# Performance work log

Measured on AMD Instinct MI355X. Metric: run time of the kernel, lower is better.

Reference implementation:

```python
import jax, jax.numpy as jnp
import numpy as np

B, N, C, H = 4, 1024, 768, 12
D = C // H  # head_dim = 64


def setup_inputs() -> dict:
    key = jax.random.key(0)
    ks = jax.random.split(key, 6)
    x = jax.random.normal(ks[0], (B, N, C), dtype=jnp.float32)
    W_qkv = jax.random.normal(ks[1], (C, 3 * C), dtype=jnp.float32) * (C ** -0.5)
    b_qkv = jnp.zeros((3 * C,), dtype=jnp.float32)
    scale = jnp.asarray(D ** -0.5, dtype=jnp.float32)       # learnable scalar in torch
    riem_scale = jnp.asarray(D ** -0.5, dtype=jnp.float32)  # learnable scalar in torch
    # 1x1 Conv2d(2H -> H) == channel-mixing matrix [H, 2H] + bias [H]
    W_conv = jax.random.normal(ks[2], (H, 2 * H), dtype=jnp.float32) * ((2 * H) ** -0.5)
    b_conv = jnp.zeros((H,), dtype=jnp.float32)
    W_proj = jax.random.normal(ks[3], (C, C), dtype=jnp.float32) * (C ** -0.5)
    b_proj = jnp.zeros((C,), dtype=jnp.float32)
    return dict(x=x, W_qkv=W_qkv, b_qkv=b_qkv, scale=scale, riem_scale=riem_scale,
                W_conv=W_conv, b_conv=b_conv, W_proj=W_proj, b_proj=b_proj)


def reference(x, W_qkv, b_qkv, scale, riem_scale, W_conv, b_conv, W_proj, b_proj):
    Bx, Nx, Cx = x.shape
    Hh = W_conv.shape[0]
    d = Cx // Hh
    # qkv projection -> [3, B, H, N, d]
    qkv = (x @ W_qkv + b_qkv).reshape(Bx, Nx, 3, Hh, d).transpose(2, 0, 3, 1, 4)
    q, k, v = qkv[0], qkv[1], qkv[2]
    # standard scaled dot-product scores [B, H, N, N]
    attn = jnp.einsum('bhnd,bhmd->bhnm', q, k) * scale
    # covariance-Frobenius (Riemannian) scores: center along feature dim, then
    # <q_c q_c^T, k_c k_c^T>_F = (q_c . k_c)^2 pairwise
    qc = q - q.mean(axis=-1, keepdims=True)
    kc = k - k.mean(axis=-1, keepdims=True)
    attn_riem = jnp.einsum('bhnd,bhmd->bhnm', qc, kc) ** 2 * riem_scale
    # concat along head/channel dim -> [B, 2H, N, N], then 1x1 conv channel mix
    cat = jnp.concatenate([attn, attn_riem], axis=1)
    mixed = jnp.einsum('bcnm,oc->bonm', cat, W_conv) + b_conv[None, :, None, None]
    attn_ = jax.nn.softmax(mixed, axis=-1)  # [B, H, N, N]
    out = jnp.einsum('bhnm,bhmd->bhnd', attn_, v)
    out = out.transpose(0, 2, 1, 3).reshape(Bx, Nx, Cx)
    return out @ W_proj + b_proj, attn_
```

## Files before the change

kernel.cpp:

```cpp
#include <hip/hip_runtime.h>
#include <cstddef>
#include <cstdint>

#define B_ 4
#define N_ 1024
#define C_ 768
#define H_ 12
#define D_ 64

typedef __attribute__((ext_vector_type(8))) short bf16x8;
typedef __attribute__((ext_vector_type(4))) short s16x4;
typedef __attribute__((ext_vector_type(4))) float f32x4;
typedef __attribute__((ext_vector_type(2))) float f32x2;

#define MFMA16(a_, b_, c_) __builtin_amdgcn_mfma_f32_16x16x32_bf16((a_), (b_), (c_), 0, 0, 0)
#define GLLDS16(gp_, lp_) __builtin_amdgcn_global_load_lds( \
    (const __attribute__((address_space(1))) unsigned int*)(gp_), \
    (__attribute__((address_space(3))) unsigned int*)(lp_), 16, 0, 0)

__device__ __forceinline__ unsigned short f2bf(float f) {
  unsigned int u = __float_as_uint(f);
  u += 0x7fffu + ((u >> 16) & 1u);
  return (unsigned short)(u >> 16);
}
__device__ __forceinline__ float bf2f(unsigned short b) {
  return __uint_as_float(((unsigned int)b) << 16);
}

__global__ __launch_bounds__(256) void k_prep(const float* __restrict__ x,
                                              short* __restrict__ xhi, short* __restrict__ xlo,
                                              const float* __restrict__ Wq,
                                              short* __restrict__ Wthi, short* __restrict__ Wtlo,
                                              const float* __restrict__ Wp,
                                              short* __restrict__ Wpthi, short* __restrict__ Wptlo) {
  __shared__ float tile[32][33];
  const int f = blockIdx.x;
  const int t = threadIdx.x;
  if (f < 1536) {
    const size_t i = ((size_t)f * 256 + t) * 8;
    float4 a = *reinterpret_cast<const float4*>(&x[i]);
    float4 b = *reinterpret_cast<const float4*>(&x[i + 4]);
    float v[8] = {a.x, a.y, a.z, a.w, b.x, b.y, b.z, b.w};
    bf16x8 hi, lo;
#pragma unroll
    for (int j = 0; j < 8; ++j) {
      unsigned short h = f2bf(v[j]);
      hi[j] = (short)h;
      lo[j] = (short)f2bf(v[j] - bf2f(h));
    }
    *reinterpret_cast<bf16x8*>(&xhi[i]) = hi;
    *reinterpret_cast<bf16x8*>(&xlo[i]) = lo;
    return;
  }
  const float* W;
  short *Thi, *Tlo;
  int Kd, Nn, bx, by;
  if (f < 3264) {
    const int local = f - 1536;
    W = Wq; Thi = Wthi; Tlo = Wtlo; Kd = 768; Nn = 2304;
    bx = local % 72; by = local / 72;
  } else {
    const int local = f - 3264;
    W = Wp; Thi = Wpthi; Tlo = Wptlo; Kd = 768; Nn = 768;
    bx = local % 24; by = local / 24;
  }
  const int k0 = by * 32, n0 = bx * 32;
  const int r = t >> 3, cq = (t & 7) * 4;
  float4 v = *reinterpret_cast<const float4*>(&W[(size_t)(k0 + r) * Nn + n0 + cq]);
  tile[r][cq + 0] = v.x; tile[r][cq + 1] = v.y;
  tile[r][cq + 2] = v.z; tile[r][cq + 3] = v.w;
  __syncthreads();
  const int nrow = t >> 3, kq = (t & 7) * 4;
  s16x4 hi, lo;
#pragma unroll
  for (int i = 0; i < 4; ++i) {
    float fv = tile[kq + i][nrow];
    unsigned short h = f2bf(fv);
    hi[i] = (short)h;
    lo[i] = (short)f2bf(fv - bf2f(h));
  }
  *reinterpret_cast<s16x4*>(&Thi[(size_t)(n0 + nrow) * Kd + k0 + kq]) = hi;
  *reinterpret_cast<s16x4*>(&Tlo[(size_t)(n0 + nrow) * Kd + k0 + kq]) = lo;
}

__global__ __launch_bounds__(256) void k_fold(const float* __restrict__ Wc,
                                              const float* __restrict__ scale_p,
                                              const float* __restrict__ riem_p,
                                              float* __restrict__ Wfold) {
  const int t = threadIdx.x;
  const float scale = scale_p[0], riem = riem_p[0];
  for (int i = t; i < 288; i += 256)
    Wfold[i] = Wc[i] * (((i % 24) < 12) ? scale : riem);
}

__global__ __launch_bounds__(256) void k_gemm(const short* __restrict__ Ahi,
                                              const short* __restrict__ Alo,
                                              const short* __restrict__ Bhi,
                                              const short* __restrict__ Blo,
                                              const float* __restrict__ bias,
                                              float* __restrict__ Cout,
                                              int M, int Nn, int Kd) {
  __shared__ __align__(16) short sA[2][128 * 32];
  __shared__ __align__(16) short sB[2][64 * 32];
  const int tid = threadIdx.x;
  const int wv = tid >> 6, l = tid & 63;
  const int lr = l & 15, lg = l >> 4;
  const int row0 = blockIdx.y * 128;
  const int col0 = blockIdx.x * 64;
  const int wr = (wv >> 1) * 64;
  const int wc = (wv & 1) * 32;
  const int ar = tid >> 2, ac = tid & 3;
  f32x4 acc[4][2];
#pragma unroll
  for (int i = 0; i < 4; ++i)
#pragma unroll
    for (int j = 0; j < 2; ++j) acc[i][j] = (f32x4){0.f, 0.f, 0.f, 0.f};

  for (int k0 = 0; k0 < Kd; k0 += 32) {
#pragma unroll
    for (int j = 0; j < 2; ++j) {
      const int row = j * 64 + ar;
      const int cc = ac ^ ((row >> 1) & 3);
      const size_t so = (size_t)(row0 + row) * Kd + k0 + cc * 8;
      GLLDS16(Ahi + so, &sA[0][(j * 256 + (wv << 6)) * 8]);
      GLLDS16(Alo + so, &sA[1][(j * 256 + (wv << 6)) * 8]);
    }
    {
      const int row = ar;
      const int cc = ac ^ ((row >> 1) & 3);
      const size_t so = (size_t)(col0 + row) * Kd + k0 + cc * 8;
      GLLDS16(Bhi + so, &sB[0][(wv << 6) * 8]);
      GLLDS16(Blo + so, &sB[1][(wv << 6) * 8]);
    }
    __syncthreads();
    bf16x8 afh[4], afl[4], bfh[2], bfl[2];
#pragma unroll
    for (int ti = 0; ti < 4; ++ti) {
      const int row = wr + ti * 16 + lr;
      const int pc = lg ^ ((row >> 1) & 3);
      afh[ti] = *reinterpret_cast<const bf16x8*>(&sA[0][row * 32 + pc * 8]);
      afl[ti] = *reinterpret_cast<const bf16x8*>(&sA[1][row * 32 + pc * 8]);
    }
#pragma unroll
    for (int tj = 0; tj < 2; ++tj) {
      const int row = wc + tj * 16 + lr;
      const int pc = lg ^ ((row >> 1) & 3);
      bfh[tj] = *reinterpret_cast<const bf16x8*>(&sB[0][row * 32 + pc * 8]);
      bfl[tj] = *reinterpret_cast<const bf16x8*>(&sB[1][row * 32 + pc * 8]);
    }
#pragma unroll
    for (int ti = 0; ti < 4; ++ti)
#pragma unroll
      for (int tj = 0; tj < 2; ++tj) {
        acc[ti][tj] = MFMA16(afh[ti], bfh[tj], acc[ti][tj]);
        acc[ti][tj] = MFMA16(afl[ti], bfh[tj], acc[ti][tj]);
        acc[ti][tj] = MFMA16(afh[ti], bfl[tj], acc[ti][tj]);
      }
    __syncthreads();
  }
#pragma unroll
  for (int ti = 0; ti < 4; ++ti)
#pragma unroll
    for (int tj = 0; tj < 2; ++tj) {
      const int col = col0 + wc + tj * 16 + lr;
      const float bb = bias[col];
#pragma unroll
      for (int r = 0; r < 4; ++r) {
        const int row = row0 + wr + ti * 16 + lg * 4 + r;
        Cout[(size_t)row * Nn + col] = acc[ti][tj][r] + bb;
      }
    }
}

__global__ __launch_bounds__(256) void k_gemm128(const short* __restrict__ Ahi,
                                                 const short* __restrict__ Alo,
                                                 const short* __restrict__ Bhi,
                                                 const short* __restrict__ Blo,
                                                 const float* __restrict__ bias,
                                                 float* __restrict__ Cout,
                                                 int M, int Nn, int Kd) {
  __shared__ __align__(16) short sA[2][128 * 32];
  __shared__ __align__(16) short sB[2][128 * 32];
  const int tid = threadIdx.x;
  const int wv = tid >> 6, l = tid & 63;
  const int lr = l & 15, lg = l >> 4;
  const int row0 = blockIdx.y * 128;
  const int col0 = blockIdx.x * 128;
  const int wr = (wv >> 1) * 64;
  const int wc = (wv & 1) * 64;
  const int ar = tid >> 2, ac = tid & 3;
  f32x4 acc[4][4];
#pragma unroll
  for (int i = 0; i < 4; ++i)
#pragma unroll
    for (int j = 0; j < 4; ++j) acc[i][j] = (f32x4){0.f, 0.f, 0.f, 0.f};

  for (int k0 = 0; k0 < Kd; k0 += 32) {
#pragma unroll
    for (int j = 0; j < 2; ++j) {
      const int row = j * 64 + ar;
      const int cc = ac ^ ((row >> 1) & 3);
      const size_t ao = (size_t)(row0 + row) * Kd + k0 + cc * 8;
      const size_t bo = (size_t)(col0 + row) * Kd + k0 + cc * 8;
      GLLDS16(Ahi + ao, &sA[0][(j * 256 + (wv << 6)) * 8]);
      GLLDS16(Alo + ao, &sA[1][(j * 256 + (wv << 6)) * 8]);
      GLLDS16(Bhi + bo, &sB[0][(j * 256 + (wv << 6)) * 8]);
      GLLDS16(Blo + bo, &sB[1][(j * 256 + (wv << 6)) * 8]);
    }
    __syncthreads();
    bf16x8 afh[4], afl[4], bfh[4], bfl[4];
#pragma unroll
    for (int ti = 0; ti < 4; ++ti) {
      const int row = wr + ti * 16 + lr;
      const int pc = lg ^ ((row >> 1) & 3);
      afh[ti] = *reinterpret_cast<const bf16x8*>(&sA[0][row * 32 + pc * 8]);
      afl[ti] = *reinterpret_cast<const bf16x8*>(&sA[1][row * 32 + pc * 8]);
    }
#pragma unroll
    for (int tj = 0; tj < 4; ++tj) {
      const int row = wc + tj * 16 + lr;
      const int pc = lg ^ ((row >> 1) & 3);
      bfh[tj] = *reinterpret_cast<const bf16x8*>(&sB[0][row * 32 + pc * 8]);
      bfl[tj] = *reinterpret_cast<const bf16x8*>(&sB[1][row * 32 + pc * 8]);
    }
#pragma unroll
    for (int ti = 0; ti < 4; ++ti)
#pragma unroll
      for (int tj = 0; tj < 4; ++tj) {
        acc[ti][tj] = MFMA16(afh[ti], bfh[tj], acc[ti][tj]);
        acc[ti][tj] = MFMA16(afl[ti], bfh[tj], acc[ti][tj]);
        acc[ti][tj] = MFMA16(afh[ti], bfl[tj], acc[ti][tj]);
      }
    __syncthreads();
  }
#pragma unroll
  for (int ti = 0; ti < 4; ++ti)
#pragma unroll
    for (int tj = 0; tj < 4; ++tj) {
      const int col = col0 + wc + tj * 16 + lr;
      const float bb = bias[col];
#pragma unroll
      for (int r = 0; r < 4; ++r) {
        const int row = row0 + wr + ti * 16 + lg * 4 + r;
        Cout[(size_t)row * Nn + col] = acc[ti][tj][r] + bb;
      }
    }
}

__global__ __launch_bounds__(256) void k_qkv_post(const float* __restrict__ qkvf,
                                                  short* __restrict__ Qhi, short* __restrict__ Qlo,
                                                  short* __restrict__ KChi, short* __restrict__ KClo,
                                                  short* __restrict__ Vt,
                                                  float* __restrict__ Qm, float* __restrict__ Km) {
  __shared__ unsigned short lvh[64][33];
  const int b = blockIdx.z, h = blockIdx.y, n0 = blockIdx.x * 32;
  const int t = threadIdx.x;
  const int row = t >> 3, d0 = (t & 7) * 8;
  const int n = n0 + row;
  const float* base = qkvf + ((size_t)(b * 1024 + n)) * 2304 + h * 64 + d0;
  const size_t qko = ((size_t)(b * H_ + h) * N_ + n) * D_ + d0;

#pragma unroll
  for (int part = 0; part < 2; ++part) {
    float4 a = *reinterpret_cast<const float4*>(base + part * 768);
    float4 c = *reinterpret_cast<const float4*>(base + part * 768 + 4);
    float v[8] = {a.x, a.y, a.z, a.w, c.x, c.y, c.z, c.w};
    float s = v[0] + v[1] + v[2] + v[3] + v[4] + v[5] + v[6] + v[7];
#pragma unroll
    for (int off = 1; off < 8; off <<= 1) s += __shfl_xor(s, off);
    const float mean = s * (1.0f / 64.0f);
    if ((t & 7) == 0) (part ? Km : Qm)[(size_t)(b * H_ + h) * N_ + n] = mean;
    const float sub = part ? mean : 0.0f;
    bf16x8 hi, lo;
#pragma unroll
    for (int j = 0; j < 8; ++j) {
      const float fv = v[j] - sub;
      unsigned short hh = f2bf(fv);
      hi[j] = (short)hh;
      lo[j] = (short)f2bf(fv - bf2f(hh));
    }
    *reinterpret_cast<bf16x8*>((part ? KChi : Qhi) + qko) = hi;
    *reinterpret_cast<bf16x8*>((part ? KClo : Qlo) + qko) = lo;
  }
  {
    float4 a = *reinterpret_cast<const float4*>(base + 1536);
    float4 c = *reinterpret_cast<const float4*>(base + 1536 + 4);
    float v[8] = {a.x, a.y, a.z, a.w, c.x, c.y, c.z, c.w};
#pragma unroll
    for (int j = 0; j < 8; ++j) lvh[d0 + j][row] = f2bf(v[j]);
  }
  __syncthreads();
  const int d = t >> 2, c = t & 3;
  bf16x8 vh;
#pragma unroll
  for (int i = 0; i < 8; ++i) vh[i] = (short)lvh[d][c * 8 + i];
  const size_t vo = ((size_t)(b * H_ + h) * D_ + d) * N_ + n0 + c * 8;
  *reinterpret_cast<bf16x8*>(Vt + vo) = vh;
}

__global__ __launch_bounds__(256, 2) void k_scores(
    const short* __restrict__ Qhi, const short* __restrict__ Qlo,
    const short* __restrict__ KChi, const short* __restrict__ KClo,
    const float* __restrict__ Qm, const float* __restrict__ Km,
    const float* __restrict__ Wfold, float* __restrict__ logits,
    float2* __restrict__ stats) {
  __shared__ __align__(16) short sCh[2][32 * 64];
  __shared__ __align__(16) short sCl[2][32 * 64];
  __shared__ float sQm[12][64];
  __shared__ float sKm[12][32];

  const int t = threadIdx.x;
  const int b = blockIdx.z;
  const int n0 = blockIdx.y * 64, m0 = blockIdx.x * 32;
  const int wv = t >> 6, l = t & 63;
  const int lr = l & 15, lg = l >> 4;
  const size_t bh0 = (size_t)b * H_;

  for (int i = t; i < 768; i += 256)
    sQm[i >> 6][i & 63] = Qm[(bh0 + (i >> 6)) * N_ + n0 + (i & 63)];
  for (int i = t; i < 384; i += 256)
    sKm[i >> 5][i & 31] = Km[(bh0 + (i >> 5)) * N_ + m0 + (i & 31)];

  const int srow = t >> 3;
  const int scs = (t & 7) ^ (srow & 7);
  const size_t csrc = (bh0 * N_ + m0 + srow) * D_ + scs * 8;
  const size_t hstep = (size_t)N_ * D_;
  const int nb = n0 + wv * 16;
  const size_t qsrc = (bh0 * N_ + nb + lr) * D_ + lg * 8;

  GLLDS16(KChi + csrc, &sCh[0][wv * 512]);
  GLLDS16(KClo + csrc, &sCl[0][wv * 512]);
  bf16x8 qh0 = *reinterpret_cast<const bf16x8*>(Qhi + qsrc);
  bf16x8 qh1 = *reinterpret_cast<const bf16x8*>(Qhi + qsrc + 32);
  bf16x8 ql0 = *reinterpret_cast<const bf16x8*>(Qlo + qsrc);
  bf16x8 ql1 = *reinterpret_cast<const bf16x8*>(Qlo + qsrc + 32);

  f32x2 aA01[12], aA23[12], aB01[12], aB23[12];
#pragma unroll
  for (int o = 0; o < 12; ++o) {
    aA01[o] = (f32x2){0.f, 0.f}; aA23[o] = (f32x2){0.f, 0.f};
    aB01[o] = (f32x2){0.f, 0.f}; aB23[o] = (f32x2){0.f, 0.f};
  }

  const int browA = lr, browB = 16 + lr;
  const int aiA0 = browA * 64 + ((lg + 0) ^ (browA & 7)) * 8;
  const int aiA1 = browA * 64 + ((lg + 4) ^ (browA & 7)) * 8;
  const int aiB0 = browB * 64 + ((lg + 0) ^ (browB & 7)) * 8;
  const int aiB1 = browB * 64 + ((lg + 4) ^ (browB & 7)) * 8;
  __syncthreads();

  int buf = 0;
#pragma unroll 2
  for (int h = 0; h < H_; ++h) {
    bf16x8 nqh0, nqh1, nql0, nql1;
    if (h < 11) {
      const size_t cs = csrc + (size_t)(h + 1) * hstep;
      GLLDS16(KChi + cs, &sCh[buf ^ 1][wv * 512]);
      GLLDS16(KClo + cs, &sCl[buf ^ 1][wv * 512]);
      const size_t qs = qsrc + (size_t)(h + 1) * hstep;
      nqh0 = *reinterpret_cast<const bf16x8*>(Qhi + qs);
      nqh1 = *reinterpret_cast<const bf16x8*>(Qhi + qs + 32);
      nql0 = *reinterpret_cast<const bf16x8*>(Qlo + qs);
      nql1 = *reinterpret_cast<const bf16x8*>(Qlo + qs + 32);
    }
    const bf16x8 chA0 = *reinterpret_cast<const bf16x8*>(&sCh[buf][aiA0]);
    const bf16x8 chA1 = *reinterpret_cast<const bf16x8*>(&sCh[buf][aiA1]);
    const bf16x8 clA0 = *reinterpret_cast<const bf16x8*>(&sCl[buf][aiA0]);
    const bf16x8 clA1 = *reinterpret_cast<const bf16x8*>(&sCl[buf][aiA1]);
    const bf16x8 chB0 = *reinterpret_cast<const bf16x8*>(&sCh[buf][aiB0]);
    const bf16x8 chB1 = *reinterpret_cast<const bf16x8*>(&sCh[buf][aiB1]);
    const bf16x8 clB0 = *reinterpret_cast<const bf16x8*>(&sCl[buf][aiB0]);
    const bf16x8 clB1 = *reinterpret_cast<const bf16x8*>(&sCl[buf][aiB1]);

    f32x4 uaA = {0.f, 0.f, 0.f, 0.f}, ubA = {0.f, 0.f, 0.f, 0.f};
    f32x4 uaB = {0.f, 0.f, 0.f, 0.f}, ubB = {0.f, 0.f, 0.f, 0.f};
    uaA = MFMA16(qh0, chA0, uaA);  ubA = MFMA16(qh1, chA1, ubA);
    uaB = MFMA16(qh0, chB0, uaB);  ubB = MFMA16(qh1, chB1, ubB);
    uaA = MFMA16(qh0, clA0, uaA);  ubA = MFMA16(qh1, clA1, ubA);
    uaB = MFMA16(qh0, clB0, uaB);  ubB = MFMA16(qh1, clB1, ubB);
    uaA = MFMA16(ql0, chA0, uaA);  ubA = MFMA16(ql1, chA1, ubA);
    uaB = MFMA16(ql0, chB0, uaB);  ubB = MFMA16(ql1, chB1, ubB);

    const float4 qm4 = *reinterpret_cast<const float4*>(&sQm[h][wv * 16 + lg * 4]);
    const float kmA = 64.0f * sKm[h][lr];
    const float kmB = 64.0f * sKm[h][16 + lr];
    const f32x2 qm01 = {qm4.x, qm4.y};
    const f32x2 qm23 = {qm4.z, qm4.w};
    const f32x2 uA01 = {uaA[0] + ubA[0], uaA[1] + ubA[1]};
    const f32x2 uA23 = {uaA[2] + ubA[2], uaA[3] + ubA[3]};
    const f32x2 uB01 = {uaB[0] + ubB[0], uaB[1] + ubB[1]};
    const f32x2 uB23 = {uaB[2] + ubB[2], uaB[3] + ubB[3]};
    const f32x2 svA01 = kmA * qm01 + uA01;
    const f32x2 svA23 = kmA * qm23 + uA23;
    const f32x2 svB01 = kmB * qm01 + uB01;
    const f32x2 svB23 = kmB * qm23 + uB23;
    const f32x2 u2A01 = uA01 * uA01;
    const f32x2 u2A23 = uA23 * uA23;
    const f32x2 u2B01 = uB01 * uB01;
    const f32x2 u2B23 = uB23 * uB23;
#pragma unroll
    for (int o = 0; o < 12; ++o) {
      const float we = Wfold[o * 24 + h];
      const float wr = Wfold[o * 24 + 12 + h];
      aA01[o] = aA01[o] + we * svA01 + wr * u2A01;
      aA23[o] = aA23[o] + we * svA23 + wr * u2A23;
      aB01[o] = aB01[o] + we * svB01 + wr * u2B01;
      aB23[o] = aB23[o] + we * svB23 + wr * u2B23;
    }
    __syncthreads();
    buf ^= 1;
    if (h < 11) { qh0 = nqh0; qh1 = nqh1; ql0 = nql0; ql1 = nql1; }
  }

#pragma unroll
  for (int o = 0; o < 12; ++o) {
    float* dst = &logits[((bh0 + o) * N_ + nb) * N_ + m0 + lr];
    dst[(size_t)(lg * 4 + 0) * N_] = aA01[o][0];
    dst[(size_t)(lg * 4 + 1) * N_] = aA01[o][1];
    dst[(size_t)(lg * 4 + 2) * N_] = aA23[o][0];
    dst[(size_t)(lg * 4 + 3) * N_] = aA23[o][1];
    dst[(size_t)(lg * 4 + 0) * N_ + 16] = aB01[o][0];
    dst[(size_t)(lg * 4 + 1) * N_ + 16] = aB01[o][1];
    dst[(size_t)(lg * 4 + 2) * N_ + 16] = aB23[o][0];
    dst[(size_t)(lg * 4 + 3) * N_ + 16] = aB23[o][1];
  }
#pragma unroll
  for (int o = 0; o < 12; ++o) {
    float avA[4] = {aA01[o][0], aA01[o][1], aA23[o][0], aA23[o][1]};
    float avB[4] = {aB01[o][0], aB01[o][1], aB23[o][0], aB23[o][1]};
    float M4[4], S4[4];
#pragma unroll
    for (int r = 0; r < 4; ++r) {
      float mxA = avA[r], mxB = avB[r];
      mxA = fmaxf(mxA, __shfl_xor(mxA, 1)); mxB = fmaxf(mxB, __shfl_xor(mxB, 1));
      mxA = fmaxf(mxA, __shfl_xor(mxA, 2)); mxB = fmaxf(mxB, __shfl_xor(mxB, 2));
      mxA = fmaxf(mxA, __shfl_xor(mxA, 4)); mxB = fmaxf(mxB, __shfl_xor(mxB, 4));
      mxA = fmaxf(mxA, __shfl_xor(mxA, 8)); mxB = fmaxf(mxB, __shfl_xor(mxB, 8));
      const float M = fmaxf(mxA, mxB);
      float eA = __expf(avA[r] - M);
      float eB = __expf(avB[r] - M);
      float e = eA + eB;
      e += __shfl_xor(e, 1);
      e += __shfl_xor(e, 2);
      e += __shfl_xor(e, 4);
      e += __shfl_xor(e, 8);
      M4[r] = M; S4[r] = e;
    }
    if (lr < 4) {
      const int n = nb + lg * 4 + lr;
      stats[(((size_t)b * 12 + o) * 32 + blockIdx.x) * 1024 + n] = make_float2(M4[lr], S4[lr]);
    }
  }
}

__global__ __launch_bounds__(256) void k_pvsm(float* __restrict__ attn,
                                              const float2* __restrict__ stats,
                                              const short* __restrict__ Vt,
                                              short* __restrict__ ohi,
                                              short* __restrict__ olo) {
  __shared__ __align__(16) short sPhi[64 * 64];
  __shared__ __align__(16) short sPlo[64 * 64];
  __shared__ __align__(16) short sV[2][64 * 64];
  __shared__ float sM[64], sIS[64];
  const int flat = blockIdx.x + blockIdx.y * 16 + blockIdx.z * 192;
  const int swz = (flat & 7) * 96 + (flat >> 3);
  const int b = swz / 192;
  const int rem = swz - b * 192;
  const int o = rem >> 4;
  const int n0 = (rem & 15) * 64;
  const int bo = b * H_ + o;
  const int t = threadIdx.x;
  const int wv = t >> 6, l = t & 63;
  const int lr = l & 15, lg = l >> 4;
  const int nsub = wv * 16;

  const int vr0 = t >> 3, vr1 = vr0 + 32;
  const int vc0 = (t & 7) ^ (vr0 & 7);
  const int vc1 = (t & 7) ^ (vr1 & 7);
  const size_t vbase = (size_t)bo * D_ * N_;
  const size_t vs0 = vbase + (size_t)vr0 * N_ + vc0 * 8;
  const size_t vs1 = vbase + (size_t)vr1 * N_ + vc1 * 8;

  GLLDS16(Vt + vs0, &sV[0][(wv * 64) * 8]);
  GLLDS16(Vt + vs1, &sV[0][(wv * 64 + 256) * 8]);

  if (t < 64) {
    const int n = n0 + t;
    const float2* sp = stats + ((size_t)bo * 32) * 1024 + n;
    float M = -3.0e38f, S = 0.f;
    for (int seg = 0; seg < 32; ++seg) {
      const float2 p = sp[(size_t)seg * 1024];
      if (p.x > M) {
        S = S * __expf(M - p.x) + p.y;
        M = p.x;
      } else {
        S += p.y * __expf(p.x - M);
      }
    }
    sM[t] = M;
    sIS[t] = 1.0f / S;
  }

  const int prow = t >> 3, c0 = (t & 7) * 8;
  float* lrowA = attn + ((size_t)bo * N_ + n0 + prow) * N_;
  float* lrowB = attn + ((size_t)bo * N_ + n0 + prow + 32) * N_;
  const int pofsA = prow * 64 + (((t & 7) ^ (prow & 7)) * 8);
  const int pofsB = pofsA + 32 * 64;

  const int arow = nsub + lr;
  const int ai0 = arow * 64 + (((lg + 0) ^ (arow & 7)) * 8);
  const int ai1 = arow * 64 + (((lg + 4) ^ (arow & 7)) * 8);

  f32x4 acc[4];
#pragma unroll
  for (int dt = 0; dt < 4; ++dt) acc[dt] = (f32x4){0.f, 0.f, 0.f, 0.f};
  __syncthreads();

  for (int mc = 0; mc < 16; ++mc) {
    const int m0 = mc * 64;
    if (mc < 15) {
      const int nb2 = (mc + 1) & 1;
      GLLDS16(Vt + vs0 + m0 + 64, &sV[nb2][(wv * 64) * 8]);
      GLLDS16(Vt + vs1 + m0 + 64, &sV[nb2][(wv * 64 + 256) * 8]);
    }
    const float MrA = sM[prow], iSA = sIS[prow];
    const float MrB = sM[prow + 32], iSB = sIS[prow + 32];
    float4 laA = *reinterpret_cast<const float4*>(&lrowA[m0 + c0]);
    float4 lbA = *reinterpret_cast<const float4*>(&lrowA[m0 + c0 + 4]);
    float4 laB = *reinterpret_cast<const float4*>(&lrowB[m0 + c0]);
    float4 lbB = *reinterpret_cast<const float4*>(&lrowB[m0 + c0 + 4]);
    float pA[8], pB[8];
    pA[0] = __expf(laA.x - MrA) * iSA; pA[1] = __expf(laA.y - MrA) * iSA;
    pA[2] = __expf(laA.z - MrA) * iSA; pA[3] = __expf(laA.w - MrA) * iSA;
    pA[4] = __expf(lbA.x - MrA) * iSA; pA[5] = __expf(lbA.y - MrA) * iSA;
    pA[6] = __expf(lbA.z - MrA) * iSA; pA[7] = __expf(lbA.w - MrA) * iSA;
    pB[0] = __expf(laB.x - MrB) * iSB; pB[1] = __expf(laB.y - MrB) * iSB;
    pB[2] = __expf(laB.z - MrB) * iSB; pB[3] = __expf(laB.w - MrB) * iSB;
    pB[4] = __expf(lbB.x - MrB) * iSB; pB[5] = __expf(lbB.y - MrB) * iSB;
    pB[6] = __expf(lbB.z - MrB) * iSB; pB[7] = __expf(lbB.w - MrB) * iSB;
    float4 oaA = {pA[0], pA[1], pA[2], pA[3]};
    float4 obA = {pA[4], pA[5], pA[6], pA[7]};
    float4 oaB = {pB[0], pB[1], pB[2], pB[3]};
    float4 obB = {pB[4], pB[5], pB[6], pB[7]};
    *reinterpret_cast<float4*>(&lrowA[m0 + c0]) = oaA;
    *reinterpret_cast<float4*>(&lrowA[m0 + c0 + 4]) = obA;
    *reinterpret_cast<float4*>(&lrowB[m0 + c0]) = oaB;
    *reinterpret_cast<float4*>(&lrowB[m0 + c0 + 4]) = obB;
    bf16x8 phiA, ploA, phiB, ploB;
#pragma unroll
    for (int j = 0; j < 8; ++j) {
      unsigned short hA = f2bf(pA[j]);
      phiA[j] = (short)hA;
      ploA[j] = (short)f2bf(pA[j] - bf2f(hA));
      unsigned short hB = f2bf(pB[j]);
      phiB[j] = (short)hB;
      ploB[j] = (short)f2bf(pB[j] - bf2f(hB));
    }
    *reinterpret_cast<bf16x8*>(&sPhi[pofsA]) = phiA;
    *reinterpret_cast<bf16x8*>(&sPlo[pofsA]) = ploA;
    *reinterpret_cast<bf16x8*>(&sPhi[pofsB]) = phiB;
    *reinterpret_cast<bf16x8*>(&sPlo[pofsB]) = ploB;
    __syncthreads();

    const int cur = mc & 1;
    const bf16x8 pah0 = *reinterpret_cast<const bf16x8*>(&sPhi[ai0]);
    const bf16x8 pah1 = *reinterpret_cast<const bf16x8*>(&sPhi[ai1]);
    const bf16x8 pal0 = *reinterpret_cast<const bf16x8*>(&sPlo[ai0]);
    const bf16x8 pal1 = *reinterpret_cast<const bf16x8*>(&sPlo[ai1]);
#pragma unroll
    for (int dt = 0; dt < 4; ++dt) {
      const int drow = dt * 16 + lr;
      const bf16x8 vh0 = *reinterpret_cast<const bf16x8*>(&sV[cur][drow * 64 + (((lg + 0) ^ (drow & 7)) * 8)]);
      const bf16x8 vh1 = *reinterpret_cast<const bf16x8*>(&sV[cur][drow * 64 + (((lg + 4) ^ (drow & 7)) * 8)]);
      acc[dt] = MFMA16(pah0, vh0, acc[dt]);
      acc[dt] = MFMA16(pal0, vh0, acc[dt]);
      acc[dt] = MFMA16(pah1, vh1, acc[dt]);
      acc[dt] = MFMA16(pal1, vh1, acc[dt]);
    }
    __syncthreads();
  }
#pragma unroll
  for (int dt = 0; dt < 4; ++dt) {
    const int d = dt * 16 + lr;
#pragma unroll
    for (int r = 0; r < 4; ++r) {
      const int n = n0 + nsub + lg * 4 + r;
      const float val = acc[dt][r];
      const unsigned short hh = f2bf(val);
      const size_t oo = (size_t)(b * 1024 + n) * 768 + o * 64 + d;
      ohi[oo] = (short)hh;
      olo[oo] = (short)f2bf(val - bf2f(hh));
    }
  }
}

extern "C" void kernel_launch(void* const* d_in, const int* in_sizes, int n_in,
                              void* d_out, int out_size, void* d_ws, size_t ws_size,
                              hipStream_t stream) {
  (void)in_sizes; (void)n_in; (void)out_size; (void)ws_size;
  const float* x      = (const float*)d_in[0];
  const float* W_qkv  = (const float*)d_in[1];
  const float* b_qkv  = (const float*)d_in[2];
  const float* scale  = (const float*)d_in[3];
  const float* riem   = (const float*)d_in[4];
  const float* W_conv = (const float*)d_in[5];
  const float* W_proj = (const float*)d_in[7];
  const float* b_proj = (const float*)d_in[8];

  float* out_final = (float*)d_out;
  float* attn_out  = out_final + (size_t)B_ * N_ * C_;

  char* w = (char*)d_ws;
  short* xhi  = (short*)w;
  short* xlo  = xhi + 3145728;
  short* Wthi = (short*)(w + 12582912);
  short* Wtlo = Wthi + 1769472;
  short* Wpthi = (short*)(w + 19660800);
  short* Wptlo = Wpthi + 589824;
  float* qkvf = (float*)(w + 22020096);
  short* Qhi  = (short*)(w + 59768832);
  short* Qlo  = Qhi + 3145728;
  short* KChi = Qlo + 3145728;
  short* KClo = KChi + 3145728;
  short* Vt = xhi;
  float* Wfold = (float*)Wthi;
  float* Qm = (float*)((char*)Wthi + 8192);
  float* Km = (float*)((char*)Wthi + 8192 + 196608);
  float2* stats = (float2*)((char*)qkvf + 12582912);

  short* ohi = Qhi;
  short* olo = Qlo;

  k_prep<<<dim3(3840), 256, 0, stream>>>(x, xhi, xlo, W_qkv, Wthi, Wtlo, W_proj, Wpthi, Wptlo);
  k_gemm128<<<dim3(18, 32), 256, 0, stream>>>(xhi, xlo, Wthi, Wtlo, b_qkv, qkvf, 4096, 2304, 768);
  k_fold<<<dim3(1), 256, 0, stream>>>(W_conv, scale, riem, Wfold);
  k_qkv_post<<<dim3(32, 12, 4), 256, 0, stream>>>(qkvf, Qhi, Qlo, KChi, KClo, Vt, Qm, Km);
  k_scores<<<dim3(32, 16, 4), 256, 0, stream>>>(Qhi, Qlo, KChi, KClo, Qm, Km, Wfold, attn_out, stats);
  k_pvsm<<<dim3(16, 12, 4), 256, 0, stream>>>(attn_out, stats, Vt, ohi, olo);
  k_gemm<<<dim3(12, 32), 256, 0, stream>>>(ohi, olo, Wpthi, Wptlo, b_proj, out_final, 4096, 768, 768);
}
```

Before: 348.4 us.

## Store mixed logits as fp16 offsets in attn buffer, reconstruct in-place in PV

The logits kernel now writes each logit as an fp16 value relative to its per-segment row max into the first half of each attn row, halving logit write and read traffic. The PV/softmax kernel stores per-segment max offsets in fp16 in LDS, reads the fp16 logits, and iterates column chunks in reverse so the fp32 probabilities written back to the same row do not overwrite unread fp16 data. The probability store is also moved after the barrier. This risks precision loss from fp16 logit storage and depends on ordering across threads to avoid in-place aliasing hazards.

```diff
diff --git a/kernel.cpp b/kernel.cpp
--- a/kernel.cpp
+++ b/kernel.cpp
@@ -25,6 +25,17 @@
 }
 __device__ __forceinline__ float bf2f(unsigned short b) {
   return __uint_as_float(((unsigned int)b) << 16);
+}
+__device__ __forceinline__ short f2h(float f) {
+  _Float16 h = (_Float16)f;
+  short s;
+  __builtin_memcpy(&s, &h, 2);
+  return s;
+}
+__device__ __forceinline__ float h2f(short s) {
+  _Float16 h;
+  __builtin_memcpy(&h, &s, 2);
+  return (float)h;
 }
 
 __global__ __launch_bounds__(256) void k_prep(const float* __restrict__ x,
@@ -414,18 +425,6 @@
 
 #pragma unroll
   for (int o = 0; o < 12; ++o) {
-    float* dst = &logits[((bh0 + o) * N_ + nb) * N_ + m0 + lr];
-    dst[(size_t)(lg * 4 + 0) * N_] = aA01[o][0];
-    dst[(size_t)(lg * 4 + 1) * N_] = aA01[o][1];
-    dst[(size_t)(lg * 4 + 2) * N_] = aA23[o][0];
-    dst[(size_t)(lg * 4 + 3) * N_] = aA23[o][1];
-    dst[(size_t)(lg * 4 + 0) * N_ + 16] = aB01[o][0];
-    dst[(size_t)(lg * 4 + 1) * N_ + 16] = aB01[o][1];
-    dst[(size_t)(lg * 4 + 2) * N_ + 16] = aB23[o][0];
-    dst[(size_t)(lg * 4 + 3) * N_ + 16] = aB23[o][1];
-  }
-#pragma unroll
-  for (int o = 0; o < 12; ++o) {
     float avA[4] = {aA01[o][0], aA01[o][1], aA23[o][0], aA23[o][1]};
     float avB[4] = {aB01[o][0], aB01[o][1], aB23[o][0], aB23[o][1]};
     float M4[4], S4[4];
@@ -446,6 +445,12 @@
       e += __shfl_xor(e, 8);
       M4[r] = M; S4[r] = e;
     }
+#pragma unroll
+    for (int r = 0; r < 4; ++r) {
+      short* rowp = (short*)(logits + ((bh0 + o) * N_ + nb + lg * 4 + r) * (size_t)N_);
+      rowp[m0 + lr] = f2h(avA[r] - M4[r]);
+      rowp[m0 + 16 + lr] = f2h(avB[r] - M4[r]);
+    }
     if (lr < 4) {
       const int n = nb + lg * 4 + lr;
       stats[(((size_t)b * 12 + o) * 32 + blockIdx.x) * 1024 + n] = make_float2(M4[lr], S4[lr]);
@@ -461,7 +466,8 @@
   __shared__ __align__(16) short sPhi[64 * 64];
   __shared__ __align__(16) short sPlo[64 * 64];
   __shared__ __align__(16) short sV[2][64 * 64];
-  __shared__ float sM[64], sIS[64];
+  __shared__ float sIS[64];
+  __shared__ short sMseg16[64 * 32];
   const int flat = blockIdx.x + blockIdx.y * 16 + blockIdx.z * 192;
   const int swz = (flat & 7) * 96 + (flat >> 3);
   const int b = swz / 192;
@@ -481,8 +487,8 @@
   const size_t vs0 = vbase + (size_t)vr0 * N_ + vc0 * 8;
   const size_t vs1 = vbase + (size_t)vr1 * N_ + vc1 * 8;
 
-  GLLDS16(Vt + vs0, &sV[0][(wv * 64) * 8]);
-  GLLDS16(Vt + vs1, &sV[0][(wv * 64 + 256) * 8]);
+  GLLDS16(Vt + vs0 + 960, &sV[1][(wv * 64) * 8]);
+  GLLDS16(Vt + vs1 + 960, &sV[1][(wv * 64 + 256) * 8]);
 
   if (t < 64) {
     const int n = n0 + t;
@@ -497,8 +503,9 @@
         S += p.y * __expf(p.x - M);
       }
     }
-    sM[t] = M;
     sIS[t] = 1.0f / S;
+    for (int seg = 0; seg < 32; ++seg)
+      sMseg16[t * 32 + seg] = f2h(sp[(size_t)seg * 1024].x - M);
   }
 
   const int prow = t >> 3, c0 = (t & 7) * 8;
@@ -516,28 +523,41 @@
   for (int dt = 0; dt < 4; ++dt) acc[dt] = (f32x4){0.f, 0.f, 0.f, 0.f};
   __syncthreads();
 
-  for (int mc = 0; mc < 16; ++mc) {
+  for (int mc = 15; mc >= 0; --mc) {
     const int m0 = mc * 64;
-    if (mc < 15) {
-      const int nb2 = (mc + 1) & 1;
-      GLLDS16(Vt + vs0 + m0 + 64, &sV[nb2][(wv * 64) * 8]);
-      GLLDS16(Vt + vs1 + m0 + 64, &sV[nb2][(wv * 64 + 256) * 8]);
-    }
-    const float MrA = sM[prow], iSA = sIS[prow];
-    const float MrB = sM[prow + 32], iSB = sIS[prow + 32];
-    float4 laA = *reinterpret_cast<const float4*>(&lrowA[m0 + c0]);
-    float4 lbA = *reinterpret_cast<const float4*>(&lrowA[m0 + c0 + 4]);
-    float4 laB = *reinterpret_cast<const float4*>(&lrowB[m0 + c0]);
-    float4 lbB = *reinterpret_cast<const float4*>(&lrowB[m0 + c0 + 4]);
+    if (mc > 0) {
+      const int nb2 = (mc - 1) & 1;
+      GLLDS16(Vt + vs0 + m0 - 64, &sV[nb2][(wv * 64) * 8]);
+      GLLDS16(Vt + vs1 + m0 - 64, &sV[nb2][(wv * 64 + 256) * 8]);
+    }
+    const int sidx = mc * 2 + ((t & 7) >> 2);
+    const float ofsA = h2f(sMseg16[prow * 32 + sidx]);
+    const float ofsB = h2f(sMseg16[(prow + 32) * 32 + sidx]);
+    const float iSA = sIS[prow], iSB = sIS[prow + 32];
+    const bf16x8 rA = *reinterpret_cast<const bf16x8*>(&((const short*)lrowA)[m0 + c0]);
+    const bf16x8 rB = *reinterpret_cast<const bf16x8*>(&((const short*)lrowB)[m0 + c0]);
     float pA[8], pB[8];
-    pA[0] = __expf(laA.x - MrA) * iSA; pA[1] = __expf(laA.y - MrA) * iSA;
-    pA[2] = __expf(laA.z - MrA) * iSA; pA[3] = __expf(laA.w - MrA) * iSA;
-    pA[4] = __expf(lbA.x - MrA) * iSA; pA[5] = __expf(lbA.y - MrA) * iSA;
-    pA[6] = __expf(lbA.z - MrA) * iSA; pA[7] = __expf(lbA.w - MrA) * iSA;
-    pB[0] = __expf(laB.x - MrB) * iSB; pB[1] = __expf(laB.y - MrB) * iSB;
-    pB[2] = __expf(laB.z - MrB) * iSB; pB[3] = __expf(laB.w - MrB) * iSB;
-    pB[4] = __expf(lbB.x - MrB) * iSB; pB[5] = __expf(lbB.y - MrB) * iSB;
-    pB[6] = __expf(lbB.z - MrB) * iSB; pB[7] = __expf(lbB.w - MrB) * iSB;
+#pragma unroll
+    for (int j = 0; j < 8; ++j) {
+      pA[j] = __expf(h2f(rA[j]) + ofsA) * iSA;
+      pB[j] = __expf(h2f(rB[j]) + ofsB) * iSB;
+    }
+    bf16x8 phiA, ploA, phiB, ploB;
+#pragma unroll
+    for (int j = 0; j < 8; ++j) {
+      unsigned short hA = f2bf(pA[j]);
+      phiA[j] = (short)hA;
+      ploA[j] = (short)f2bf(pA[j] - bf2f(hA));
+      unsigned short hB = f2bf(pB[j]);
+      phiB[j] = (short)hB;
+      ploB[j] = (short)f2bf(pB[j] - bf2f(hB));
+    }
+    *reinterpret_cast<bf16x8*>(&sPhi[pofsA]) = phiA;
+    *reinterpret_cast<bf16x8*>(&sPlo[pofsA]) = ploA;
+    *reinterpret_cast<bf16x8*>(&sPhi[pofsB]) = phiB;
+    *reinterpret_cast<bf16x8*>(&sPlo[pofsB]) = ploB;
+    __syncthreads();
+
     float4 oaA = {pA[0], pA[1], pA[2], pA[3]};
     float4 obA = {pA[4], pA[5], pA[6], pA[7]};
     float4 oaB = {pB[0], pB[1], pB[2], pB[3]};
@@ -546,21 +566,6 @@
     *reinterpret_cast<float4*>(&lrowA[m0 + c0 + 4]) = obA;
     *reinterpret_cast<float4*>(&lrowB[m0 + c0]) = oaB;
     *reinterpret_cast<float4*>(&lrowB[m0 + c0 + 4]) = obB;
-    bf16x8 phiA, ploA, phiB, ploB;
-#pragma unroll
-    for (int j = 0; j < 8; ++j) {
-      unsigned short hA = f2bf(pA[j]);
-      phiA[j] = (short)hA;
-      ploA[j] = (short)f2bf(pA[j] - bf2f(hA));
-      unsigned short hB = f2bf(pB[j]);
-      phiB[j] = (short)hB;
-      ploB[j] = (short)f2bf(pB[j] - bf2f(hB));
-    }
-    *reinterpret_cast<bf16x8*>(&sPhi[pofsA]) = phiA;
-    *reinterpret_cast<bf16x8*>(&sPlo[pofsA]) = ploA;
-    *reinterpret_cast<bf16x8*>(&sPhi[pofsB]) = phiB;
-    *reinterpret_cast<bf16x8*>(&sPlo[pofsB]) = ploB;
-    __syncthreads();
 
     const int cur = mc & 1;
     const bf16x8 pah0 = *reinterpret_cast<const bf16x8*>(&sPhi[ai0]);
```

Result: faster. 313.0 us (-10.2%).
